# Performance work log

Hardware: AMD Instinct MI355X
Metric: run time of the kernel (lower is better)

Reference implementation:

```python
import jax, jax.numpy as jnp
import numpy as np

N_EMBD = 1024
BLOCK_SIZE = 2048
ATTN_SPAN = 256
LN_EPS = 1e-5


def _band_mask(T, span, dtype):
    ones = jnp.ones((T, T), dtype=dtype)
    # tril(.,0) * (1 - tril(.,-span)) -> causal band of width `span`
    return jnp.tril(ones, 0) * (1.0 - jnp.tril(ones, -span))


def setup_inputs() -> dict:
    key = jax.random.key(0)
    k_x, k_w, k_b, k_lw = jax.random.split(key, 4)
    B, T, C = 4, BLOCK_SIZE, N_EMBD
    x = jax.random.normal(k_x, (B, T, C), dtype=jnp.float32)
    # qkv_net: Linear(C, 3C) with bias (torch default)
    lim = 1.0 / np.sqrt(C)
    W_qkv = jax.random.uniform(k_w, (C, 3 * C), minval=-lim, maxval=lim, dtype=jnp.float32)
    b_qkv = jax.random.uniform(k_b, (3 * C,), minval=-lim, maxval=lim, dtype=jnp.float32)
    ln_w = jnp.ones((C,), dtype=jnp.float32)
    ln_b = jnp.zeros((C,), dtype=jnp.float32)
    return {"x": x, "W_qkv": W_qkv, "b_qkv": b_qkv, "ln_w": ln_w, "ln_b": ln_b}


def _layer_norm(h, w, b):
    mu = jnp.mean(h, axis=-1, keepdims=True)
    var = jnp.var(h, axis=-1, keepdims=True)
    return (h - mu) * jax.lax.rsqrt(var + LN_EPS) * w + b


def reference(x, W_qkv, b_qkv, ln_w, ln_b):
    B, T, C = x.shape
    qkv = x @ W_qkv + b_qkv  # [B,T,3C]
    q, k, v = jnp.split(qkv, 3, axis=-1)
    scale = np.sqrt(C * ATTN_SPAN).astype(np.float32)
    scores = jnp.einsum('bid,bjd->bij', q, k) / scale  # [B,T,T]
    scores = scores * _band_mask(T, ATTN_SPAN, x.dtype)[None, :, :]
    out = jnp.einsum('bij,bjd->bid', scores, v)  # [B,T,C]
    return _layer_norm(out, ln_w, ln_b)
```

## Files before the change

### kernel.cpp

```cpp
#include <hip/hip_runtime.h>
#include <cstdint>
#include <cstddef>

#define N_EMBD 1024
#define T_SEQ  2048
#define NBATCH 4
#define SPAN   256
#define C3     3072

typedef float  floatx4 __attribute__((ext_vector_type(4)));
typedef __bf16 bf16x8  __attribute__((ext_vector_type(8)));

__device__ inline unsigned short f2bf(float f) {
    union { float f; unsigned u; } x; x.f = f;
    unsigned u = x.u;
    unsigned r = (u + 0x7fffu + ((u >> 16) & 1u)) >> 16;
    return (unsigned short)r;
}

typedef __attribute__((address_space(1))) const void GVOID;
typedef __attribute__((address_space(3))) void LVOID;
__device__ inline void gl2lds16(const void* g, void* l) {
    __builtin_amdgcn_global_load_lds((GVOID*)g, (LVOID*)l, 16, 0, 0);
}

__device__ inline void stage128x32(const unsigned short* g, size_t stride,
                                   unsigned short* lds, int lane, int wave) {
    const int r     = wave * 16 + (lane >> 2);
    const int chunk = (lane & 3) ^ ((r >> 1) & 3);
    const unsigned short* src = g + (size_t)r * stride + chunk * 8;
    gl2lds16(src,               &lds[(wave * 16) * 32]);
    gl2lds16(src + 64 * stride, &lds[(64 + wave * 16) * 32]);
}

__device__ inline void stage64x64(const unsigned short* g, size_t stride,
                                  unsigned short* lds, int lane, int wave) {
#pragma unroll
    for (int rnd = 0; rnd < 2; rnd++) {
        const int r = rnd * 32 + wave * 8 + (lane >> 3);
        const int chunk = (lane & 7) ^ (r & 7);
        gl2lds16(g + (size_t)r * stride + chunk * 8, &lds[(rnd * 32 + wave * 8) * 64]);
    }
}

__device__ inline void stage128x64(const unsigned short* g, size_t stride,
                                   unsigned short* lds, int lane, int wave) {
#pragma unroll
    for (int rnd = 0; rnd < 4; rnd++) {
        const int r = rnd * 32 + wave * 8 + (lane >> 3);
        const int chunk = (lane & 7) ^ (r & 7);
        gl2lds16(g + (size_t)r * stride + chunk * 8, &lds[(rnd * 32 + wave * 8) * 64]);
    }
}

__global__ __launch_bounds__(256) void k_prep(const float* __restrict__ x,
                                              unsigned short* __restrict__ Xb,
                                              const float* __restrict__ W,
                                              unsigned short* __restrict__ WbT) {
    __shared__ unsigned short t[32][33];
    if (blockIdx.x < 8192) {
        int i = (blockIdx.x * 256 + threadIdx.x) * 4;
        float4 v = *(const float4*)(x + i);
        ushort4 o;
        o.x = f2bf(v.x); o.y = f2bf(v.y); o.z = f2bf(v.z); o.w = f2bf(v.w);
        *(ushort4*)(Xb + i) = o;
    } else {
        int bid = blockIdx.x - 8192;
        int k0 = (bid & 31) * 32, n0 = (bid >> 5) * 32;
        int tx = threadIdx.x & 31, ty = threadIdx.x >> 5;
#pragma unroll
        for (int i = 0; i < 4; i++) {
            int k = k0 + ty + i * 8;
            t[ty + i * 8][tx] = f2bf(W[(size_t)k * C3 + n0 + tx]);
        }
        __syncthreads();
#pragma unroll
        for (int i = 0; i < 4; i++) {
            int n = n0 + ty + i * 8;
            WbT[(size_t)n * N_EMBD + k0 + tx] = t[tx][ty + i * 8];
        }
    }
}

__global__ __launch_bounds__(256) void k_gemm(const unsigned short* __restrict__ Xb,
                                              const unsigned short* __restrict__ WbT,
                                              const float* __restrict__ bqkv,
                                              unsigned short* __restrict__ QK,
                                              unsigned short* __restrict__ Vt) {
    __shared__ unsigned short As[4096];
    __shared__ unsigned short Bs[4096];
    const int tid = threadIdx.x, lane = tid & 63, wave = tid >> 6;
    const int bx = blockIdx.x, m0 = blockIdx.y * 128;
    const bool isV = (bx >= 16);
    const int n0 = isV ? (2048 + (bx - 16) * 128) : (bx * 128);
    const int wr = wave >> 1, wc = wave & 1;

    floatx4 acc[4][4] = {};

    const unsigned short* gA = (isV ? WbT + (size_t)n0 * N_EMBD : Xb  + (size_t)m0 * N_EMBD);
    const unsigned short* gB = (isV ? Xb  + (size_t)m0 * N_EMBD : WbT + (size_t)n0 * N_EMBD);
    const int qk = ((lane >> 4) ^ ((lane >> 1) & 3)) * 8;
    const int ra = wr * 64 + (lane & 15);
    const int rb = wc * 64 + (lane & 15);

    for (int k0 = 0; k0 < N_EMBD; k0 += 32) {
        stage128x32(gA + k0, N_EMBD, As, lane, wave);
        stage128x32(gB + k0, N_EMBD, Bs, lane, wave);
        __syncthreads();
        bf16x8 a[4], b[4];
#pragma unroll
        for (int mi = 0; mi < 4; mi++) a[mi] = *(const bf16x8*)&As[(ra + mi * 16) * 32 + qk];
#pragma unroll
        for (int ni = 0; ni < 4; ni++) b[ni] = *(const bf16x8*)&Bs[(rb + ni * 16) * 32 + qk];
#pragma unroll
        for (int mi = 0; mi < 4; mi++)
#pragma unroll
            for (int ni = 0; ni < 4; ni++)
                acc[mi][ni] = __builtin_amdgcn_mfma_f32_16x16x32_bf16(a[mi], b[ni], acc[mi][ni], 0, 0, 0);
        __syncthreads();
    }

    const int cn = lane & 15, q = lane >> 4;
    unsigned short* base = isV ? Vt : QK;
    const int rowbase = isV ? (((m0 >> 11) << 10) + (n0 - 2048)) : m0;
    const int colbase = isV ? (m0 & 2047) : n0;
#pragma unroll
    for (int mi = 0; mi < 4; mi++) {
#pragma unroll
        for (int r = 0; r < 4; r++) {
            const int arow = wr * 64 + mi * 16 + q * 4 + r;
            unsigned short* dst = base + (size_t)(rowbase + arow) * 2048 + colbase;
#pragma unroll
            for (int ni = 0; ni < 4; ni++) {
                const int acol = wc * 64 + ni * 16 + cn;
                const float bias = bqkv[n0 + (isV ? arow : acol)];
                dst[acol] = f2bf(acc[mi][ni][r] + bias);
            }
        }
    }
}

__global__ __launch_bounds__(256) void k_scores(const unsigned short* __restrict__ QK,
                                                unsigned short* __restrict__ S) {
    const int logical = (blockIdx.x & 7) * 80 + (blockIdx.x >> 3);
    const int jj = logical % 5;
    const int qb = (logical / 5) & 31;
    const int b  = logical / 160;
    const int jb = qb - 4 + jj;
    if (jb < 0) return;

    __shared__ unsigned short Qs[2][4096];
    __shared__ unsigned short Ks[2][4096];
    const int tid = threadIdx.x, lane = tid & 63, wave = tid >> 6;
    const int wr = wave >> 1, wc = wave & 1;
    const int n15 = lane & 15, q = lane >> 4;

    floatx4 acc[2][2] = {};

    const unsigned short* gQ = QK + ((size_t)(b * T_SEQ + qb * 64)) * 2048;
    const unsigned short* gK = QK + ((size_t)(b * T_SEQ + jb * 64)) * 2048 + 1024;

    for (int k0 = 0; k0 < N_EMBD; k0 += 128) {
        stage64x64(gQ + k0,      2048, Qs[0], lane, wave);
        stage64x64(gQ + k0 + 64, 2048, Qs[1], lane, wave);
        stage64x64(gK + k0,      2048, Ks[0], lane, wave);
        stage64x64(gK + k0 + 64, 2048, Ks[1], lane, wave);
        __syncthreads();
#pragma unroll
        for (int h = 0; h < 2; h++) {
#pragma unroll
            for (int s = 0; s < 2; s++) {
                bf16x8 a[2], bbf[2];
#pragma unroll
                for (int mi = 0; mi < 2; mi++) {
                    const int row = wr * 32 + mi * 16 + n15;
                    a[mi] = *(const bf16x8*)&Qs[h][row * 64 + (((s * 4 + q) ^ (row & 7)) * 8)];
                }
#pragma unroll
                for (int ni = 0; ni < 2; ni++) {
                    const int row = wc * 32 + ni * 16 + n15;
                    bbf[ni] = *(const bf16x8*)&Ks[h][row * 64 + (((s * 4 + q) ^ (row & 7)) * 8)];
                }
#pragma unroll
                for (int mi = 0; mi < 2; mi++)
#pragma unroll
                    for (int ni = 0; ni < 2; ni++)
                        acc[mi][ni] = __builtin_amdgcn_mfma_f32_16x16x32_bf16(a[mi], bbf[ni], acc[mi][ni], 0, 0, 0);
            }
        }
        __syncthreads();
    }

    unsigned short* Sb = S + (((size_t)(b * 32 + qb) * 5 + jj) << 12);
#pragma unroll
    for (int mi = 0; mi < 2; mi++)
#pragma unroll
        for (int ni = 0; ni < 2; ni++)
#pragma unroll
            for (int r = 0; r < 4; r++) {
                const int il = wr * 32 + mi * 16 + q * 4 + r;
                const int jl = wc * 32 + ni * 16 + n15;
                const int gi = qb * 64 + il, gj = jb * 64 + jl;
                const float v = ((gj <= gi) && (gj > gi - SPAN)) ? acc[mi][ni][r] * (1.0f / 512.0f) : 0.0f;
                Sb[il * 64 + jl] = f2bf(v);
            }
}

__global__ __launch_bounds__(256) void k_sv(const unsigned short* __restrict__ S,
                                            const unsigned short* __restrict__ Vt,
                                            float* __restrict__ out) {
    const int logical = (blockIdx.x & 7) * 128 + (blockIdx.x >> 3);
    const int cg = logical & 7;
    const int qb = (logical >> 3) & 31;
    const int b  = logical >> 8;
    const int c0 = cg * 128;

    __shared__ unsigned short Ss[2][4096];
    __shared__ unsigned short Vs[2][8192];
    const int tid = threadIdx.x, lane = tid & 63, wave = tid >> 6;
    const int wr = wave >> 1, wc = wave & 1;
    const int n15 = lane & 15, q = lane >> 4;

    floatx4 acc[2][4] = {};

    const size_t vbase = ((size_t)(b * 1024 + c0)) * 2048;
    const size_t sbase = ((size_t)(b * 32 + qb) * 5) << 12;

    for (int j0 = 0; j0 < 5; j0 += 2) {
        const int nv = (j0 < 4) ? 2 : 1;
        bool val[2] = {false, false};
#pragma unroll
        for (int t = 0; t < 2; t++) {
            if (t < nv && (qb - 4 + j0 + t) >= 0) {
                val[t] = true;
                stage64x64 (S + sbase + ((size_t)(j0 + t) << 12), 64, Ss[t], lane, wave);
                stage128x64(Vt + vbase + (size_t)(qb - 4 + j0 + t) * 64, 2048, Vs[t], lane, wave);
            }
        }
        __syncthreads();
#pragma unroll
        for (int t = 0; t < 2; t++) {
            if (!val[t]) continue;
#pragma unroll
            for (int s = 0; s < 2; s++) {
                bf16x8 a[2], bbf[4];
#pragma unroll
                for (int mi = 0; mi < 2; mi++) {
                    const int row = wr * 32 + mi * 16 + n15;
                    a[mi] = *(const bf16x8*)&Ss[t][row * 64 + (((s * 4 + q) ^ (row & 7)) * 8)];
                }
#pragma unroll
                for (int ni = 0; ni < 4; ni++) {
                    const int row = wc * 64 + ni * 16 + n15;
                    bbf[ni] = *(const bf16x8*)&Vs[t][row * 64 + (((s * 4 + q) ^ (row & 7)) * 8)];
                }
#pragma unroll
                for (int mi = 0; mi < 2; mi++)
#pragma unroll
                    for (int ni = 0; ni < 4; ni++)
                        acc[mi][ni] = __builtin_amdgcn_mfma_f32_16x16x32_bf16(a[mi], bbf[ni], acc[mi][ni], 0, 0, 0);
            }
        }
        __syncthreads();
    }

#pragma unroll
    for (int mi = 0; mi < 2; mi++)
#pragma unroll
        for (int ni = 0; ni < 4; ni++)
#pragma unroll
            for (int r = 0; r < 4; r++) {
                const int il = wr * 32 + mi * 16 + q * 4 + r;
                const int cl = wc * 64 + ni * 16 + n15;
                out[((size_t)(b * T_SEQ + qb * 64 + il)) * N_EMBD + c0 + cl] = acc[mi][ni][r];
            }
}

__global__ __launch_bounds__(256) void k_ln(float* __restrict__ out,
                                            const float* __restrict__ w,
                                            const float* __restrict__ bias) {
    __shared__ float red[8];
    const int t = threadIdx.x;
    float* p = out + (size_t)blockIdx.x * N_EMBD;
    float4 v = ((const float4*)p)[t];
    float s  = v.x + v.y + v.z + v.w;
    float sq = v.x * v.x + v.y * v.y + v.z * v.z + v.w * v.w;
#pragma unroll
    for (int off = 32; off; off >>= 1) {
        s  += __shfl_down(s, off, 64);
        sq += __shfl_down(sq, off, 64);
    }
    const int wave = t >> 6, lane = t & 63;
    if (lane == 0) { red[wave] = s; red[4 + wave] = sq; }
    __syncthreads();
    const float ts = red[0] + red[1] + red[2] + red[3];
    const float tq = red[4] + red[5] + red[6] + red[7];
    const float mean = ts * (1.0f / N_EMBD);
    const float var  = tq * (1.0f / N_EMBD) - mean * mean;
    const float rs = rsqrtf(var + 1e-5f);
    float4 wv = ((const float4*)w)[t];
    float4 bv = ((const float4*)bias)[t];
    float4 o;
    o.x = (v.x - mean) * rs * wv.x + bv.x;
    o.y = (v.y - mean) * rs * wv.y + bv.y;
    o.z = (v.z - mean) * rs * wv.z + bv.z;
    o.w = (v.w - mean) * rs * wv.w + bv.w;
    ((float4*)p)[t] = o;
}

extern "C" void kernel_launch(void* const* d_in, const int* in_sizes, int n_in,
                              void* d_out, int out_size, void* d_ws, size_t ws_size,
                              hipStream_t stream) {
    const float* x  = (const float*)d_in[0];
    const float* W  = (const float*)d_in[1];
    const float* bq = (const float*)d_in[2];
    const float* lw = (const float*)d_in[3];
    const float* lb = (const float*)d_in[4];
    float* out = (float*)d_out;
    char* ws = (char*)d_ws;

    unsigned short* Xb   = (unsigned short*)(ws + 0);
    unsigned short* Sbuf = (unsigned short*)(ws + 0);
    unsigned short* WbT  = (unsigned short*)(ws + 16777216);
    unsigned short* QK   = (unsigned short*)(ws + 23068672);
    unsigned short* Vt   = (unsigned short*)(ws + 56623104);

    k_prep   <<<11264, 256, 0, stream>>>(x, Xb, W, WbT);
    k_gemm   <<<dim3(24, 64), 256, 0, stream>>>(Xb, WbT, bq, QK, Vt);
    k_scores <<<640,   256, 0, stream>>>(QK, Sbuf);
    k_sv     <<<1024,  256, 0, stream>>>(Sbuf, Vt, out);
    k_ln     <<<8192,  256, 0, stream>>>(out, lw, lb);
}
```

Before: 192.9 us.

## Fuse layernorm into SV kernel via atomic row stats and grid barrier

Removes the separate layernorm kernel. Each SV block reduces per-row partial sums and sums of squares across its column slice and adds them atomically into a workspace stats buffer. It then waits on a per-row-group counter until all 8 column-group blocks have contributed, and writes normalized output straight from registers. This avoids writing the unnormalized output and reading it back. In exchange it adds a memset, global atomics and a spin-wait that assumes the 8 cooperating blocks are co-resident on the GPU.

Measured after the change: 252.0 us. +30.7%, slower.

```diff
diff --git a/kernel.cpp b/kernel.cpp
--- a/kernel.cpp
+++ b/kernel.cpp
@@ -208,6 +208,10 @@
 
 __global__ __launch_bounds__(256) void k_sv(const unsigned short* __restrict__ S,
                                             const unsigned short* __restrict__ Vt,
+                                            float* __restrict__ stats,
+                                            unsigned int* __restrict__ cnt,
+                                            const float* __restrict__ lw,
+                                            const float* __restrict__ lb,
                                             float* __restrict__ out) {
     const int logical = (blockIdx.x & 7) * 128 + (blockIdx.x >> 3);
     const int cg = logical & 7;
@@ -264,48 +268,66 @@
         __syncthreads();
     }
 
+    float ps[2][4], pq[2][4];
 #pragma unroll
     for (int mi = 0; mi < 2; mi++)
 #pragma unroll
-        for (int ni = 0; ni < 4; ni++)
+        for (int r = 0; r < 4; r++) {
+            float s = 0.0f, sq = 0.0f;
+#pragma unroll
+            for (int ni = 0; ni < 4; ni++) {
+                const float v = acc[mi][ni][r];
+                s += v; sq += v * v;
+            }
+#pragma unroll
+            for (int off = 1; off < 16; off <<= 1) {
+                s  += __shfl_xor(s, off, 64);
+                sq += __shfl_xor(sq, off, 64);
+            }
+            ps[mi][r] = s; pq[mi][r] = sq;
+        }
+    if (n15 == 0) {
+#pragma unroll
+        for (int mi = 0; mi < 2; mi++)
 #pragma unroll
             for (int r = 0; r < 4; r++) {
-                const int il = wr * 32 + mi * 16 + q * 4 + r;
-                const int cl = wc * 64 + ni * 16 + n15;
-                out[((size_t)(b * T_SEQ + qb * 64 + il)) * N_EMBD + c0 + cl] = acc[mi][ni][r];
-            }
-}
-
-__global__ __launch_bounds__(256) void k_ln(float* __restrict__ out,
-                                            const float* __restrict__ w,
-                                            const float* __restrict__ bias) {
-    __shared__ float red[8];
-    const int t = threadIdx.x;
-    float* p = out + (size_t)blockIdx.x * N_EMBD;
-    float4 v = ((const float4*)p)[t];
-    float s  = v.x + v.y + v.z + v.w;
-    float sq = v.x * v.x + v.y * v.y + v.z * v.z + v.w * v.w;
-#pragma unroll
-    for (int off = 32; off; off >>= 1) {
-        s  += __shfl_down(s, off, 64);
-        sq += __shfl_down(sq, off, 64);
-    }
-    const int wave = t >> 6, lane = t & 63;
-    if (lane == 0) { red[wave] = s; red[4 + wave] = sq; }
+                const size_t row = (size_t)(b * T_SEQ + qb * 64 + wr * 32 + mi * 16 + q * 4 + r);
+                atomicAdd(&stats[row * 2 + 0], ps[mi][r]);
+                atomicAdd(&stats[row * 2 + 1], pq[mi][r]);
+            }
+    }
     __syncthreads();
-    const float ts = red[0] + red[1] + red[2] + red[3];
-    const float tq = red[4] + red[5] + red[6] + red[7];
-    const float mean = ts * (1.0f / N_EMBD);
-    const float var  = tq * (1.0f / N_EMBD) - mean * mean;
-    const float rs = rsqrtf(var + 1e-5f);
-    float4 wv = ((const float4*)w)[t];
-    float4 bv = ((const float4*)bias)[t];
-    float4 o;
-    o.x = (v.x - mean) * rs * wv.x + bv.x;
-    o.y = (v.y - mean) * rs * wv.y + bv.y;
-    o.z = (v.z - mean) * rs * wv.z + bv.z;
-    o.w = (v.w - mean) * rs * wv.w + bv.w;
-    ((float4*)p)[t] = o;
+    const int grp = b * 32 + qb;
+    if (tid == 0) {
+        __threadfence();
+        atomicAdd(&cnt[grp], 1u);
+        while (__hip_atomic_load(&cnt[grp], __ATOMIC_ACQUIRE, __HIP_MEMORY_SCOPE_AGENT) < 8u)
+            __builtin_amdgcn_s_sleep(8);
+    }
+    __syncthreads();
+
+    float wv[4], bv[4];
+#pragma unroll
+    for (int ni = 0; ni < 4; ni++) {
+        const int c = c0 + wc * 64 + ni * 16 + n15;
+        wv[ni] = lw[c]; bv[ni] = lb[c];
+    }
+#pragma unroll
+    for (int mi = 0; mi < 2; mi++)
+#pragma unroll
+        for (int r = 0; r < 4; r++) {
+            const int il = wr * 32 + mi * 16 + q * 4 + r;
+            const size_t row = (size_t)(b * T_SEQ + qb * 64 + il);
+            const float ts = __hip_atomic_load(&stats[row * 2 + 0], __ATOMIC_RELAXED, __HIP_MEMORY_SCOPE_AGENT);
+            const float tq = __hip_atomic_load(&stats[row * 2 + 1], __ATOMIC_RELAXED, __HIP_MEMORY_SCOPE_AGENT);
+            const float mean = ts * (1.0f / N_EMBD);
+            const float var  = tq * (1.0f / N_EMBD) - mean * mean;
+            const float rs = rsqrtf(var + 1e-5f);
+            float* po = out + row * N_EMBD + c0 + wc * 64;
+#pragma unroll
+            for (int ni = 0; ni < 4; ni++)
+                po[ni * 16 + n15] = (acc[mi][ni][r] - mean) * rs * wv[ni] + bv[ni];
+        }
 }
 
 extern "C" void kernel_launch(void* const* d_in, const int* in_sizes, int n_in,
@@ -319,15 +341,17 @@
     float* out = (float*)d_out;
     char* ws = (char*)d_ws;
 
-    unsigned short* Xb   = (unsigned short*)(ws + 0);
-    unsigned short* Sbuf = (unsigned short*)(ws + 0);
-    unsigned short* WbT  = (unsigned short*)(ws + 16777216);
-    unsigned short* QK   = (unsigned short*)(ws + 23068672);
-    unsigned short* Vt   = (unsigned short*)(ws + 56623104);
+    unsigned short* Xb    = (unsigned short*)(ws + 0);
+    unsigned short* Sbuf  = (unsigned short*)(ws + 0);
+    float*          stats = (float*)(ws + 6291456);
+    unsigned int*   cnt   = (unsigned int*)(ws + 6356992);
+    unsigned short* WbT   = (unsigned short*)(ws + 16777216);
+    unsigned short* QK    = (unsigned short*)(ws + 23068672);
+    unsigned short* Vt    = (unsigned short*)(ws + 56623104);
 
     k_prep   <<<11264, 256, 0, stream>>>(x, Xb, W, WbT);
     k_gemm   <<<dim3(24, 64), 256, 0, stream>>>(Xb, WbT, bq, QK, Vt);
+    hipMemsetAsync(ws + 6291456, 0, 66048, stream);
     k_scores <<<640,   256, 0, stream>>>(QK, Sbuf);
-    k_sv     <<<1024,  256, 0, stream>>>(Sbuf, Vt, out);
-    k_ln     <<<8192,  256, 0, stream>>>(out, lw, lb);
-}
+    k_sv     <<<1024,  256, 0, stream>>>(Sbuf, Vt, stats, cnt, lw, lb, out);
+}
```
